# Performance work log

Measured on AMD Instinct MI355X. Metric: run time of the kernel, lower is better.

The kernel has to match this reference:

```python
import jax, jax.numpy as jnp
import numpy as np
from jax import lax

KS = 5            # patch kernel size
STRIDE = 4        # patch stride / scale ratio
SHIFTS = (2, 2)   # roll shifts before patch extraction
SOFTMAX_SCALE = 10.0
MID_CH = 64
BAND_HS = 8


def same_pad(x, k, s):
    """TensorFlow-style SAME padding for kernel k, stride s (NCHW)."""
    H, W = x.shape[-2], x.shape[-1]
    oh, ow = -(-H // s), -(-W // s)
    ph = max(0, (oh - 1) * s + k - H)
    pw = max(0, (ow - 1) * s + k - W)
    return jnp.pad(x, ((0, 0), (0, 0), (ph // 2, ph - ph // 2), (pw // 2, pw - pw // 2)))


def extract_patches(x, k, s, shifts):
    """torch.nn.Unfold equivalent with SAME padding and roll -> [N, L, C, k, k]."""
    x = same_pad(x, k, s)
    x = jnp.roll(x, shifts[0], axis=2)
    x = jnp.roll(x, shifts[1], axis=3)
    p = lax.conv_general_dilated_patches(
        x, (k, k), (s, s), 'VALID', dimension_numbers=('NCHW', 'OIHW', 'NCHW'))
    N, _, Hn, Wn = p.shape
    C = x.shape[1]
    # channel ordering is (C, kh, kw) channel-slowest, matching torch unfold
    return p.reshape(N, C, k, k, Hn * Wn).transpose(0, 4, 1, 2, 3)


def conv3(x, w, b):
    """3x3 conv, padding=1, bias + LeakyReLU(0.01) (BasicBlock)."""
    y = lax.conv_general_dilated(x, w, (1, 1), [(1, 1), (1, 1)],
                                 dimension_numbers=('NCHW', 'OIHW', 'NCHW'))
    return jax.nn.leaky_relu(y + b[None, :, None, None], 0.01)


def setup_inputs() -> dict:
    key = jax.random.key(0)
    ks = jax.random.split(key, 11)
    f32 = jnp.float32
    return {
        'ms':   jax.random.normal(ks[0], (2, BAND_HS, 96, 96), f32),
        'pan':  jax.random.normal(ks[1], (2, 1, 384, 384), f32),
        'pan2': jax.random.normal(ks[2], (2, 1, 96, 96), f32),
        'wq': jax.random.normal(ks[3], (MID_CH, 1, 3, 3), f32) * 0.1,
        'bq': jax.random.normal(ks[4], (MID_CH,), f32) * 0.02,
        'wk': jax.random.normal(ks[5], (MID_CH, 1, 3, 3), f32) * 0.1,
        'bk': jax.random.normal(ks[6], (MID_CH,), f32) * 0.02,
        'wv': jax.random.normal(ks[7], (BAND_HS, BAND_HS, 3, 3), f32) * 0.1,
        'bv': jax.random.normal(ks[8], (BAND_HS,), f32) * 0.02,
        'wr': jax.random.normal(ks[9], (BAND_HS, BAND_HS, 3, 3), f32) * 0.1,
        'br': jax.random.normal(ks[10], (BAND_HS,), f32) * 0.02,
    }


def reference(ms, pan, pan2, wq, bq, wk, bk, wv, bv, wr, br):
    k_fea = conv3(pan2, wk, bk)                       # [N, mid, h, w]
    q_fea = conv3(pan, wq, bq)                        # [N, mid, H, W]
    v_fea = conv3(ms, wv, bv)                         # [N, band, h, w]

    k_patch = extract_patches(k_fea, KS, STRIDE, SHIFTS)  # [N, L, mid, ks, ks]
    v_patch = extract_patches(v_fea, KS, STRIDE, SHIFTS)  # [N, L, band, ks, ks]

    def attend(q, kp, vp):
        # q: [mid, H, W]; kp: [L, mid, ks, ks]; vp: [L, band, ks, ks]
        norms = jnp.sqrt(jnp.sum(kp * kp, axis=(1, 2, 3)))      # per-patch L2 norms
        k0 = kp / jnp.max(norms)                                # global-max normalization
        q0 = same_pad(q[None], KS, STRIDE)                      # [1, mid, Hp, Wp]
        scores = lax.conv_general_dilated(
            q0, k0, (STRIDE, STRIDE), 'VALID',
            dimension_numbers=('NCHW', 'OIHW', 'NCHW'))          # [1, L, H', W']
        attn = jax.nn.softmax(scores * SOFTMAX_SCALE, axis=1)
        # conv_transpose2d(attn, vp, stride) == dilated conv with flipped, transposed kernel
        wT = jnp.flip(vp, (2, 3)).transpose(1, 0, 2, 3)          # [band, L, ks, ks]
        out = lax.conv_general_dilated(
            attn, wT, (1, 1), [(KS - 1, KS - 1)] * 2,
            lhs_dilation=(STRIDE, STRIDE),
            dimension_numbers=('NCHW', 'OIHW', 'NCHW'))          # [1, band, Ho, Wo]
        return out[0] / 6.0

    res = jax.vmap(attend)(q_fea, k_patch, v_patch)   # [N, band, Ho, Wo]
    return conv3(res, wr, br)
```

## Files before the change

### kernel.cpp

```cpp
#include <hip/hip_runtime.h>
#include <math.h>


typedef _Float16 f16;
typedef _Float16 f16x8 __attribute__((ext_vector_type(8)));
typedef float f32x4 __attribute__((ext_vector_type(4)));

namespace csa {
constexpr int NB   = 2;
constexpr int MID  = 64;
constexpr int BAND = 8;
constexpr int HK   = 96;
constexpr int HQ   = 384;
constexpr int HQP  = 385;
constexpr int XI   = 97;
constexpr int LN   = 24;
constexpr int L    = 576;
constexpr int LP   = 640;
constexpr int PS   = 96 * 96;
constexpr int KDIM = MID * 25;
constexpr int VDIM = BAND * 25;
constexpr int MV   = 256;
constexpr int HO   = 385;
constexpr size_t QPSN = (size_t)4 * HQP * XI * MID;

constexpr int NBQ = (NB * 4 * HQP * XI + 255) / 256;
constexpr int NBC = NB * HK * HK / 256;

constexpr size_t align256(size_t x) { return (x + 255) & ~(size_t)255; }
constexpr size_t OFF_QPS  = 0;
constexpr size_t OFF_KCL  = align256(OFF_QPS + (size_t)NB*QPSN*2);
constexpr size_t OFF_VFEA = align256(OFF_KCL + (size_t)NB*HK*HK*MID*2);
constexpr size_t OFF_SC   = align256(OFF_VFEA + (size_t)NB*BAND*HK*HK*4);
constexpr size_t OFF_KM   = align256(OFF_SC   + 256);
constexpr size_t OFF_VT   = align256(OFF_KM   + (size_t)NB*LP*KDIM*2);
constexpr size_t OFF_ST   = align256(OFF_VT   + (size_t)NB*MV*L*2);
constexpr size_t OFF_AT   = align256(OFF_ST   + (size_t)NB*PS*LP*4);
constexpr size_t OFF_D    = align256(OFF_AT   + (size_t)NB*PS*L*2);
}
using namespace csa;

__device__ __forceinline__ void dev_convq(
    const float* __restrict__ in, const float* __restrict__ w,
    const float* __restrict__ b, f16* __restrict__ out, int id) {
  int total = NB * 4 * HQP * XI;
  if (id >= total) return;
  int xi = id % XI;
  int t = id / XI;
  int yp = t % HQP;
  t /= HQP;
  int f = t % 4;
  int n = t / 4;
  int xp = 4 * xi + f;
  f16* op = out + (size_t)id * MID;
  if (yp >= HQ || xp >= HQ) {
    f16x8 z = {0, 0, 0, 0, 0, 0, 0, 0};
#pragma unroll
    for (int c8 = 0; c8 < 8; ++c8) *(f16x8*)(op + c8 * 8) = z;
    return;
  }
  const float* ip = in + (size_t)n * HQ * HQ;
  float p[9];
#pragma unroll
  for (int dy = 0; dy < 3; ++dy)
#pragma unroll
    for (int dx = 0; dx < 3; ++dx) {
      int yy = yp + dy - 1, xx = xp + dx - 1;
      p[dy * 3 + dx] = (yy >= 0 && yy < HQ && xx >= 0 && xx < HQ)
                           ? ip[(size_t)yy * HQ + xx] : 0.f;
    }
#pragma unroll
  for (int c8 = 0; c8 < 8; ++c8) {
    f16x8 o;
#pragma unroll
    for (int e = 0; e < 8; ++e) {
      int co = c8 * 8 + e;
      float acc = b[co];
#pragma unroll
      for (int k = 0; k < 9; ++k) acc = fmaf(p[k], w[co * 9 + k], acc);
      o[e] = (f16)(acc > 0.f ? acc : 0.01f * acc);
    }
    *(f16x8*)(op + c8 * 8) = o;
  }
}

__device__ __forceinline__ void dev_conv_cl(
    const float* __restrict__ in, const float* __restrict__ w,
    const float* __restrict__ b, f16* __restrict__ out, int H, int id) {
  int total = NB * H * H;
  if (id >= total) return;
  int x = id % H;
  int t = id / H;
  int y = t % H;
  int n = t / H;
  f16* op = out + (size_t)id * MID;
  const float* ip = in + (size_t)n * H * H;
  float p[9];
#pragma unroll
  for (int dy = 0; dy < 3; ++dy)
#pragma unroll
    for (int dx = 0; dx < 3; ++dx) {
      int yy = y + dy - 1, xx = x + dx - 1;
      p[dy * 3 + dx] = (yy >= 0 && yy < H && xx >= 0 && xx < H)
                           ? ip[(size_t)yy * H + xx] : 0.f;
    }
#pragma unroll
  for (int c8 = 0; c8 < 8; ++c8) {
    f16x8 o;
#pragma unroll
    for (int e = 0; e < 8; ++e) {
      int co = c8 * 8 + e;
      float acc = b[co];
#pragma unroll
      for (int k = 0; k < 9; ++k) acc = fmaf(p[k], w[co * 9 + k], acc);
      o[e] = (f16)(acc > 0.f ? acc : 0.01f * acc);
    }
    *(f16x8*)(op + c8 * 8) = o;
  }
}

__device__ __forceinline__ void dev_conv8x8(
    const float* __restrict__ in, const float* __restrict__ w,
    const float* __restrict__ b, float* __restrict__ out, int H, int W,
    int id) {
  int total = NB * H * W;
  if (id >= total) return;
  int x = id % W;
  int t = id / W;
  int y = t % H;
  int n = t / H;
  const float* ip = in + (size_t)n * BAND * H * W;
  float p[BAND][9];
#pragma unroll
  for (int ci = 0; ci < BAND; ++ci)
#pragma unroll
    for (int dy = 0; dy < 3; ++dy)
#pragma unroll
      for (int dx = 0; dx < 3; ++dx) {
        int yy = y + dy - 1, xx = x + dx - 1;
        p[ci][dy * 3 + dx] = (yy >= 0 && yy < H && xx >= 0 && xx < W)
                                 ? ip[((size_t)ci * H + yy) * W + xx] : 0.f;
      }
  float* op = out + ((size_t)n * BAND * H + y) * W + x;
  for (int co = 0; co < BAND; ++co) {
    float acc = b[co];
#pragma unroll
    for (int ci = 0; ci < BAND; ++ci)
#pragma unroll
      for (int k = 0; k < 9; ++k)
        acc = fmaf(p[ci][k], w[(co * BAND + ci) * 9 + k], acc);
    acc = acc > 0.f ? acc : 0.01f * acc;
    op[(size_t)co * H * W] = acc;
  }
}

__global__ __launch_bounds__(256) void csa_convs(
    const float* __restrict__ pan, const float* __restrict__ wq,
    const float* __restrict__ bq, f16* __restrict__ qps,
    const float* __restrict__ pan2, const float* __restrict__ wk,
    const float* __restrict__ bk, f16* __restrict__ kcl,
    const float* __restrict__ ms, const float* __restrict__ wv,
    const float* __restrict__ bv, float* __restrict__ v_fea,
    float* __restrict__ maxn2) {
  const int bid = blockIdx.x;
  const int tid = threadIdx.x;
  if (bid == 0 && tid < NB) maxn2[tid] = 0.f;
  if (bid < NBQ) {
    dev_convq(pan, wq, bq, qps, bid * 256 + tid);
  } else if (bid < NBQ + NBC) {
    dev_conv_cl(pan2, wk, bk, kcl, HK, (bid - NBQ) * 256 + tid);
  } else {
    dev_conv8x8(ms, wv, bv, v_fea, HK, HK, (bid - NBQ - NBC) * 256 + tid);
  }
}

__global__ __launch_bounds__(256) void csa_build_patches(
    const f16* __restrict__ kcl, const float* __restrict__ v_fea,
    f16* __restrict__ Kmat, f16* __restrict__ Vt, float* __restrict__ maxn2) {
  int blk = blockIdx.x;
  int n = blk / LP;
  int l = blk % LP;
  int tid = threadIdx.x;
  f16* krow = Kmat + ((size_t)n * LP + l) * KDIM;
  if (l >= L) {
    f16x8 z = {0, 0, 0, 0, 0, 0, 0, 0};
    for (int ch = tid; ch < 200; ch += 256) *(f16x8*)(krow + ch * 8) = z;
    return;
  }
  int i = l / LN, j = l % LN;
  const f16* kn = kcl + (size_t)n * HK * HK * MID;
  float ss = 0.f;
  for (int ch = tid; ch < 200; ch += 256) {
    int khkw = ch >> 3;
    int c0 = (ch & 7) * 8;
    int kh = khkw / 5, kw = khkw % 5;
    int r = (4 * i + kh + 95) % 97;
    int cc = (4 * j + kw + 95) % 97;
    f16x8 v = {0, 0, 0, 0, 0, 0, 0, 0};
    if (r < HK && cc < HK)
      v = *(const f16x8*)(kn + ((size_t)r * HK + cc) * MID + c0);
#pragma unroll
    for (int e = 0; e < 8; ++e) {
      float fv = (float)v[e];
      ss += fv * fv;
    }
    *(f16x8*)(krow + ch * 8) = v;
  }
  for (int m = tid; m < MV; m += 256) {
    float v = 0.f;
    if (m < VDIM) {
      int kw = m % 5;
      int t = m / 5;
      int kh = t % 5;
      int c = t / 5;
      int r = (4 * i + kh + 95) % 97;
      int cc = (4 * j + kw + 95) % 97;
      v = (r < HK && cc < HK)
              ? v_fea[(((size_t)n * BAND + c) * HK + r) * HK + cc] : 0.f;
    }
    Vt[((size_t)n * MV + m) * L + l] = (f16)v;
  }
  __shared__ float red[256];
  red[tid] = ss;
  __syncthreads();
  for (int s = 128; s > 0; s >>= 1) {
    if (tid < s) red[tid] += red[tid + s];
    __syncthreads();
  }
  if (tid == 0)
    atomicMax((int*)&maxn2[n], __float_as_int(red[0]));
}

__device__ __forceinline__ void gl_lds16(const f16* g, f16* s) {
  __builtin_amdgcn_global_load_lds(
      (const __attribute__((address_space(1))) void*)g,
      (__attribute__((address_space(3))) void*)s, 16, 0, 0);
}

__global__ __launch_bounds__(256) void csa_gemm1(
    const f16* __restrict__ qps, const f16* __restrict__ Km,
    float* __restrict__ C) {
  __shared__ __attribute__((aligned(16))) f16 As[3 * 4096];
  __shared__ __attribute__((aligned(16))) f16 Bs[3 * 4096];
  const int tid = threadIdx.x;
  const int w = tid >> 6;
  const int l = tid & 63;
  const int q = l >> 4;
  const int r = l & 15;

  const int flat = blockIdx.x + 5 * (blockIdx.y + 72 * blockIdx.z);
  const int logical = (flat & 7) * 90 + (flat >> 3);
  const int bx = logical % 5;
  const int by = (logical / 5) % 72;
  const int nb = logical / 360;

  qps += (size_t)nb * QPSN;
  Km += (size_t)nb * LP * KDIM;
  C += (size_t)nb * (size_t)PS * L;
  const int bm = by * 128;
  const int bn = bx * 128;
  const int wm = (w >> 1) * 64;
  const int wn = (w & 1) * 64;

  f32x4 acc[4][4];
#pragma unroll
  for (int i = 0; i < 4; ++i)
#pragma unroll
    for (int j = 0; j < 4; ++j) {
      f32x4 z = {0.f, 0.f, 0.f, 0.f};
      acc[i][j] = z;
    }

  const int pg0 = bm + w * 16;
  const int y0 = pg0 / 96, x0 = pg0 % 96;
  const int pg1 = pg0 + 64;
  const int y1 = pg1 / 96, x1 = pg1 % 96;
  const int la = r * MID + q * 8;

  const f16* gb0 = Km + (size_t)(bn + w * 16 + r) * KDIM + q * 8;
  const f16* gb1 = gb0 + (size_t)64 * KDIM;
  const int am = (w >> 1) * 4;
  const int bnn = (w & 1) * 4;

  auto stage = [&](int t, int bi) {
    f16* bA = As + bi * 4096;
    f16* bB = Bs + bi * 4096;
    const int kh = t / 10;
    const int rem = t - kh * 10;
    const int kw = rem >> 1;
    const int half = rem & 1;
    const size_t u0 =
        (((size_t)(kw & 3) * HQP + (4 * y0 + kh)) * XI + x0 + (kw >> 2)) * MID;
    const size_t u1 =
        (((size_t)(kw & 3) * HQP + (4 * y1 + kh)) * XI + x1 + (kw >> 2)) * MID;
    const size_t oA = (size_t)half * 32 + la;
    gl_lds16(qps + u0 + oA, bA + w * 512);
    gl_lds16(qps + u1 + oA, bA + 2048 + w * 512);
    gl_lds16(gb0 + (size_t)t * 32, bB + w * 512);
    gl_lds16(gb1 + (size_t)t * 32, bB + 2048 + w * 512);
  };
  auto compute = [&](int bi) {
    const f16* bA = As + bi * 4096;
    const f16* bB = Bs + bi * 4096;
    f16x8 af[4], bf[4];
#pragma unroll
    for (int u = 0; u < 4; ++u) {
      af[u] = *(const f16x8*)&bA[(am + u) * 512 + q * 128 + r * 8];
      bf[u] = *(const f16x8*)&bB[(bnn + u) * 512 + q * 128 + r * 8];
    }
#pragma unroll
    for (int i = 0; i < 4; ++i)
#pragma unroll
      for (int j = 0; j < 4; ++j)
        acc[i][j] = __builtin_amdgcn_mfma_f32_16x16x32_f16(af[i], bf[j],
                                                           acc[i][j], 0, 0, 0);
  };

  stage(0, 0);
  stage(1, 1);
  int bi = 0;
  for (int t = 0; t < 48; ++t) {
    asm volatile("s_waitcnt vmcnt(4)" ::: "memory");
    __builtin_amdgcn_s_barrier();
    __builtin_amdgcn_sched_barrier(0);
    stage(t + 2, bi == 0 ? 2 : bi - 1);
    compute(bi);
    bi = (bi == 2) ? 0 : bi + 1;
  }
  asm volatile("s_waitcnt vmcnt(4)" ::: "memory");
  __builtin_amdgcn_s_barrier();
  __builtin_amdgcn_sched_barrier(0);
  compute(bi);
  bi = (bi == 2) ? 0 : bi + 1;
  asm volatile("s_waitcnt vmcnt(0)" ::: "memory");
  __builtin_amdgcn_s_barrier();
  __builtin_amdgcn_sched_barrier(0);
  compute(bi);

  const int cn = bn + wn + r;
#pragma unroll
  for (int i = 0; i < 4; ++i) {
    int rm = bm + wm + i * 16 + q * 4;
#pragma unroll
    for (int j = 0; j < 4; ++j) {
      int c = cn + j * 16;
      if (c < L) {
#pragma unroll
        for (int rr = 0; rr < 4; ++rr)
          C[(size_t)(rm + rr) * L + c] = acc[i][j][rr];
      }
    }
  }
}

__global__ __launch_bounds__(256) void csa_gemm2(
    const f16* __restrict__ Vt, const f16* __restrict__ At,
    float* __restrict__ D) {
  __shared__ __attribute__((aligned(16))) f16 As[3 * 2048];
  __shared__ __attribute__((aligned(16))) f16 Bs[3 * 4096];
  const int tid = threadIdx.x;
  const int w = tid >> 6;
  const int l = tid & 63;
  const int q = l >> 4;
  const int r = l & 15;

  const int flat = blockIdx.x + 72 * (blockIdx.y + 4 * blockIdx.z);
  const int logical = (flat & 7) * 72 + (flat >> 3);
  const int my = logical % 4;
  const int nx = (logical / 4) % 72;
  const int nb = logical / 288;

  const f16* A = Vt + (size_t)nb * MV * L;
  const f16* Bt = At + (size_t)nb * (size_t)PS * L;
  float* C = D + (size_t)nb * (size_t)MV * PS;
  const int bm = my * 64;
  const int bn = nx * 128;
  const int wm = (w >> 1) * 32;
  const int wn = (w & 1) * 64;

  f32x4 acc[2][4];
#pragma unroll
  for (int i = 0; i < 2; ++i)
#pragma unroll
    for (int j = 0; j < 4; ++j) {
      f32x4 z = {0.f, 0.f, 0.f, 0.f};
      acc[i][j] = z;
    }

  const f16* ga  = A + (size_t)(bm + w * 16 + r) * L + q * 8;
  const f16* gb0 = Bt + (size_t)(bn + w * 16 + r) * L + q * 8;
  const f16* gb1 = gb0 + (size_t)64 * L;
  const int am = (w >> 1) * 2;
  const int bnn = (w & 1) * 4;

  auto stage = [&](int t, int bi) {
    f16* bA = As + bi * 2048;
    f16* bB = Bs + bi * 4096;
    const size_t k0 = (size_t)t * 32;
    gl_lds16(ga + k0, bA + w * 512);
    gl_lds16(gb0 + k0, bB + w * 512);
    gl_lds16(gb1 + k0, bB + 2048 + w * 512);
  };
  auto compute = [&](int bi) {
    const f16* bA = As + bi * 2048;
    const f16* bB = Bs + bi * 4096;
    f16x8 af[2], bf[4];
#pragma unroll
    for (int u = 0; u < 2; ++u)
      af[u] = *(const f16x8*)&bA[(am + u) * 512 + q * 128 + r * 8];
#pragma unroll
    for (int u = 0; u < 4; ++u)
      bf[u] = *(const f16x8*)&bB[(bnn + u) * 512 + q * 128 + r * 8];
#pragma unroll
    for (int i = 0; i < 2; ++i)
#pragma unroll
      for (int j = 0; j < 4; ++j)
        acc[i][j] = __builtin_amdgcn_mfma_f32_16x16x32_f16(af[i], bf[j],
                                                           acc[i][j], 0, 0, 0);
  };

  stage(0, 0);
  stage(1, 1);
  int bi = 0;
  for (int t = 0; t < 16; ++t) {
    asm volatile("s_waitcnt vmcnt(3)" ::: "memory");
    __builtin_amdgcn_s_barrier();
    __builtin_amdgcn_sched_barrier(0);
    stage(t + 2, bi == 0 ? 2 : bi - 1);
    compute(bi);
    bi = (bi == 2) ? 0 : bi + 1;
  }
  asm volatile("s_waitcnt vmcnt(3)" ::: "memory");
  __builtin_amdgcn_s_barrier();
  __builtin_amdgcn_sched_barrier(0);
  compute(bi);
  bi = (bi == 2) ? 0 : bi + 1;
  asm volatile("s_waitcnt vmcnt(0)" ::: "memory");
  __builtin_amdgcn_s_barrier();
  __builtin_amdgcn_sched_barrier(0);
  compute(bi);

  const int cn = bn + wn + r;
#pragma unroll
  for (int i = 0; i < 2; ++i) {
    int rm = bm + wm + i * 16 + q * 4;
#pragma unroll
    for (int j = 0; j < 4; ++j)
#pragma unroll
      for (int rr = 0; rr < 4; ++rr)
        C[(size_t)(rm + rr) * PS + cn + j * 16] = acc[i][j][rr];
  }
}

__global__ __launch_bounds__(256) void csa_softmax(
    const float* __restrict__ scoresT, const float* __restrict__ maxn2,
    f16* __restrict__ attnT) {
  const int wv = threadIdx.x >> 6;
  const int lane = threadIdx.x & 63;
  const int p = blockIdx.x * 4 + wv;
  const int n = blockIdx.y;
  const float sc = 10.f * rsqrtf(maxn2[n]);
  const float* row = scoresT + ((size_t)n * PS + p) * L;
  float v[9];
  float m = -1e30f;
#pragma unroll
  for (int j = 0; j < 9; ++j) {
    v[j] = row[lane + j * 64] * sc;
    m = fmaxf(m, v[j]);
  }
#pragma unroll
  for (int off = 32; off > 0; off >>= 1) m = fmaxf(m, __shfl_xor(m, off));
  float e[9], s = 0.f;
#pragma unroll
  for (int j = 0; j < 9; ++j) {
    e[j] = __expf(v[j] - m);
    s += e[j];
  }
#pragma unroll
  for (int off = 32; off > 0; off >>= 1) s += __shfl_xor(s, off);
  const float inv = 1.f / s;
  f16* orow = attnT + ((size_t)n * PS + p) * L;
#pragma unroll
  for (int j = 0; j < 9; ++j) orow[lane + j * 64] = (f16)(e[j] * inv);
}

__global__ __launch_bounds__(256) void csa_gather_conv(
    const float* __restrict__ D, const float* __restrict__ wr,
    const float* __restrict__ br, float* __restrict__ out) {
  __shared__ float rs[BAND][18][18];
  __shared__ float wsm[BAND * BAND * 9];
  __shared__ float brs[BAND];
  const int tid = threadIdx.x;
  const int n = blockIdx.z;
  const int ty = blockIdx.y, tx = blockIdx.x;
  const float* Dn = D + (size_t)n * MV * PS;

  for (int i = tid; i < BAND * BAND * 9; i += 256) wsm[i] = wr[i];
  if (tid < BAND) brs[tid] = br[tid];

  for (int idx = tid; idx < BAND * 18 * 18; idx += 256) {
    int ci = idx / 324;
    int rem = idx - ci * 324;
    int yy = rem / 18;
    int xx = rem - yy * 18;
    int oy = ty * 16 - 1 + yy;
    int ox = tx * 16 - 1 + xx;
    float s = 0.f;
    if (oy >= 0 && oy < HO && ox >= 0 && ox < HO) {
      int kh0 = oy & 3;
      int kw0 = ox & 3;
      for (int kh = kh0; kh < 5; kh += 4) {
        int y = (oy - kh) >> 2;
        if (y < 0 || y >= 96) continue;
        for (int kw = kw0; kw < 5; kw += 4) {
          int x = (ox - kw) >> 2;
          if (x < 0 || x >= 96) continue;
          s += Dn[(size_t)(ci * 25 + kh * 5 + kw) * PS + y * 96 + x];
        }
      }
      s *= (1.f / 6.f);
    }
    rs[ci][yy][xx] = s;
  }
  __syncthreads();

  const int y = tid >> 4, x = tid & 15;
  const int oy = ty * 16 + y, ox = tx * 16 + x;
  if (oy >= HO || ox >= HO) return;
  float p[BAND][9];
#pragma unroll
  for (int ci = 0; ci < BAND; ++ci)
#pragma unroll
    for (int dy = 0; dy < 3; ++dy)
#pragma unroll
      for (int dx = 0; dx < 3; ++dx)
        p[ci][dy * 3 + dx] = rs[ci][y + dy][x + dx];
  float* op = out + ((size_t)n * BAND * HO + oy) * HO + ox;
  for (int co = 0; co < BAND; ++co) {
    float acc = brs[co];
#pragma unroll
    for (int ci = 0; ci < BAND; ++ci)
#pragma unroll
      for (int k = 0; k < 9; ++k)
        acc = fmaf(p[ci][k], wsm[(co * BAND + ci) * 9 + k], acc);
    acc = acc > 0.f ? acc : 0.01f * acc;
    op[(size_t)co * HO * HO] = acc;
  }
}

extern "C" void kernel_launch(void* const* d_in, const int* in_sizes, int n_in,
                              void* d_out, int out_size, void* d_ws,
                              size_t ws_size, hipStream_t stream) {
  const float* ms   = (const float*)d_in[0];
  const float* pan  = (const float*)d_in[1];
  const float* pan2 = (const float*)d_in[2];
  const float* wq = (const float*)d_in[3];
  const float* bq = (const float*)d_in[4];
  const float* wk = (const float*)d_in[5];
  const float* bk = (const float*)d_in[6];
  const float* wv = (const float*)d_in[7];
  const float* bv = (const float*)d_in[8];
  const float* wr = (const float*)d_in[9];
  const float* br = (const float*)d_in[10];
  float* out = (float*)d_out;

  char* ws = (char*)d_ws;
  f16*   qps   = (f16*)(ws + OFF_QPS);
  f16*   kcl   = (f16*)(ws + OFF_KCL);
  float* v_fea = (float*)(ws + OFF_VFEA);
  float* maxn2 = (float*)(ws + OFF_SC);
  f16*   Kmat  = (f16*)(ws + OFF_KM);
  f16*   Vt    = (f16*)(ws + OFF_VT);
  float* scoT  = (float*)(ws + OFF_ST);
  f16*   attnT = (f16*)(ws + OFF_AT);
  float* Dm    = (float*)(ws + OFF_D);

  dim3 b256(256);
  csa_convs<<<dim3(NBQ + 2 * NBC), b256, 0, stream>>>(
      pan, wq, bq, qps, pan2, wk, bk, kcl, ms, wv, bv, v_fea, maxn2);
  csa_build_patches<<<dim3(NB * LP), b256, 0, stream>>>(kcl, v_fea, Kmat, Vt,
                                                        maxn2);

  csa_gemm1<<<dim3(LP / 128, PS / 128, NB), b256, 0, stream>>>(qps, Kmat,
                                                               scoT);

  csa_softmax<<<dim3(PS / 4, NB), b256, 0, stream>>>(scoT, maxn2, attnT);

  csa_gemm2<<<dim3(PS / 128, MV / 64, NB), b256, 0, stream>>>(Vt, attnT, Dm);

  csa_gather_conv<<<dim3((HO + 15) / 16, (HO + 15) / 16, NB), b256, 0,
                    stream>>>(Dm, wr, br, out);
}
```

Baseline: 281.9 us.

## Fuse softmax exponentiation into second GEMM using precomputed row statistics

Replaces the softmax kernel that wrote a full f16 attention matrix with a kernel that stores only per-row max and inverse sum. The second GEMM now loads fp32 scores into registers, computes exp and converts to f16 while staging into LDS, and applies the 1/sum normalisation in the epilogue. This removes the write and re-read of the attention intermediate, but gemm2 now reads twice-as-wide fp32 data and recomputes exp for each row-block tile, with a register-staged pipeline.

```diff
diff --git a/kernel.cpp b/kernel.cpp
--- a/kernel.cpp
+++ b/kernel.cpp
@@ -35,8 +35,8 @@
 constexpr size_t OFF_KM   = align256(OFF_SC   + 256);
 constexpr size_t OFF_VT   = align256(OFF_KM   + (size_t)NB*LP*KDIM*2);
 constexpr size_t OFF_ST   = align256(OFF_VT   + (size_t)NB*MV*L*2);
-constexpr size_t OFF_AT   = align256(OFF_ST   + (size_t)NB*PS*LP*4);
-constexpr size_t OFF_D    = align256(OFF_AT   + (size_t)NB*PS*L*2);
+constexpr size_t OFF_RS   = align256(OFF_ST   + (size_t)NB*PS*LP*4);
+constexpr size_t OFF_D    = align256(OFF_RS   + (size_t)NB*PS*8);
 }
 using namespace csa;
 
@@ -353,108 +353,9 @@
   }
 }
 
-__global__ __launch_bounds__(256) void csa_gemm2(
-    const f16* __restrict__ Vt, const f16* __restrict__ At,
-    float* __restrict__ D) {
-  __shared__ __attribute__((aligned(16))) f16 As[3 * 2048];
-  __shared__ __attribute__((aligned(16))) f16 Bs[3 * 4096];
-  const int tid = threadIdx.x;
-  const int w = tid >> 6;
-  const int l = tid & 63;
-  const int q = l >> 4;
-  const int r = l & 15;
-
-  const int flat = blockIdx.x + 72 * (blockIdx.y + 4 * blockIdx.z);
-  const int logical = (flat & 7) * 72 + (flat >> 3);
-  const int my = logical % 4;
-  const int nx = (logical / 4) % 72;
-  const int nb = logical / 288;
-
-  const f16* A = Vt + (size_t)nb * MV * L;
-  const f16* Bt = At + (size_t)nb * (size_t)PS * L;
-  float* C = D + (size_t)nb * (size_t)MV * PS;
-  const int bm = my * 64;
-  const int bn = nx * 128;
-  const int wm = (w >> 1) * 32;
-  const int wn = (w & 1) * 64;
-
-  f32x4 acc[2][4];
-#pragma unroll
-  for (int i = 0; i < 2; ++i)
-#pragma unroll
-    for (int j = 0; j < 4; ++j) {
-      f32x4 z = {0.f, 0.f, 0.f, 0.f};
-      acc[i][j] = z;
-    }
-
-  const f16* ga  = A + (size_t)(bm + w * 16 + r) * L + q * 8;
-  const f16* gb0 = Bt + (size_t)(bn + w * 16 + r) * L + q * 8;
-  const f16* gb1 = gb0 + (size_t)64 * L;
-  const int am = (w >> 1) * 2;
-  const int bnn = (w & 1) * 4;
-
-  auto stage = [&](int t, int bi) {
-    f16* bA = As + bi * 2048;
-    f16* bB = Bs + bi * 4096;
-    const size_t k0 = (size_t)t * 32;
-    gl_lds16(ga + k0, bA + w * 512);
-    gl_lds16(gb0 + k0, bB + w * 512);
-    gl_lds16(gb1 + k0, bB + 2048 + w * 512);
-  };
-  auto compute = [&](int bi) {
-    const f16* bA = As + bi * 2048;
-    const f16* bB = Bs + bi * 4096;
-    f16x8 af[2], bf[4];
-#pragma unroll
-    for (int u = 0; u < 2; ++u)
-      af[u] = *(const f16x8*)&bA[(am + u) * 512 + q * 128 + r * 8];
-#pragma unroll
-    for (int u = 0; u < 4; ++u)
-      bf[u] = *(const f16x8*)&bB[(bnn + u) * 512 + q * 128 + r * 8];
-#pragma unroll
-    for (int i = 0; i < 2; ++i)
-#pragma unroll
-      for (int j = 0; j < 4; ++j)
-        acc[i][j] = __builtin_amdgcn_mfma_f32_16x16x32_f16(af[i], bf[j],
-                                                           acc[i][j], 0, 0, 0);
-  };
-
-  stage(0, 0);
-  stage(1, 1);
-  int bi = 0;
-  for (int t = 0; t < 16; ++t) {
-    asm volatile("s_waitcnt vmcnt(3)" ::: "memory");
-    __builtin_amdgcn_s_barrier();
-    __builtin_amdgcn_sched_barrier(0);
-    stage(t + 2, bi == 0 ? 2 : bi - 1);
-    compute(bi);
-    bi = (bi == 2) ? 0 : bi + 1;
-  }
-  asm volatile("s_waitcnt vmcnt(3)" ::: "memory");
-  __builtin_amdgcn_s_barrier();
-  __builtin_amdgcn_sched_barrier(0);
-  compute(bi);
-  bi = (bi == 2) ? 0 : bi + 1;
-  asm volatile("s_waitcnt vmcnt(0)" ::: "memory");
-  __builtin_amdgcn_s_barrier();
-  __builtin_amdgcn_sched_barrier(0);
-  compute(bi);
-
-  const int cn = bn + wn + r;
-#pragma unroll
-  for (int i = 0; i < 2; ++i) {
-    int rm = bm + wm + i * 16 + q * 4;
-#pragma unroll
-    for (int j = 0; j < 4; ++j)
-#pragma unroll
-      for (int rr = 0; rr < 4; ++rr)
-        C[(size_t)(rm + rr) * PS + cn + j * 16] = acc[i][j][rr];
-  }
-}
-
-__global__ __launch_bounds__(256) void csa_softmax(
+__global__ __launch_bounds__(256) void csa_rowstats(
     const float* __restrict__ scoresT, const float* __restrict__ maxn2,
-    f16* __restrict__ attnT) {
+    float2* __restrict__ rowst) {
   const int wv = threadIdx.x >> 6;
   const int lane = threadIdx.x & 63;
   const int p = blockIdx.x * 4 + wv;
@@ -470,18 +371,163 @@
   }
 #pragma unroll
   for (int off = 32; off > 0; off >>= 1) m = fmaxf(m, __shfl_xor(m, off));
-  float e[9], s = 0.f;
-#pragma unroll
-  for (int j = 0; j < 9; ++j) {
-    e[j] = __expf(v[j] - m);
-    s += e[j];
-  }
+  float s = 0.f;
+#pragma unroll
+  for (int j = 0; j < 9; ++j) s += __expf(v[j] - m);
 #pragma unroll
   for (int off = 32; off > 0; off >>= 1) s += __shfl_xor(s, off);
-  const float inv = 1.f / s;
-  f16* orow = attnT + ((size_t)n * PS + p) * L;
-#pragma unroll
-  for (int j = 0; j < 9; ++j) orow[lane + j * 64] = (f16)(e[j] * inv);
+  if (lane == 0) rowst[(size_t)n * PS + p] = make_float2(m, 1.f / s);
+}
+
+__global__ __launch_bounds__(256) void csa_gemm2f(
+    const f16* __restrict__ Vt, const float* __restrict__ scoT,
+    const float* __restrict__ maxn2, const float2* __restrict__ rowst,
+    float* __restrict__ D) {
+  __shared__ __attribute__((aligned(16))) f16 As[3 * 2048];
+  __shared__ __attribute__((aligned(16))) f16 Bs[3 * 4096];
+  const int tid = threadIdx.x;
+  const int w = tid >> 6;
+  const int lid = tid & 63;
+  const int q = lid >> 4;
+  const int r = lid & 15;
+
+  const int flat = blockIdx.x + 72 * (blockIdx.y + 4 * blockIdx.z);
+  const int logical = (flat & 7) * 72 + (flat >> 3);
+  const int my = logical % 4;
+  const int nx = (logical / 4) % 72;
+  const int nb = logical / 288;
+
+  const f16* A = Vt + (size_t)nb * MV * L;
+  const float* Sc = scoT + (size_t)nb * (size_t)PS * L;
+  const float2* rs = rowst + (size_t)nb * PS;
+  float* C = D + (size_t)nb * (size_t)MV * PS;
+  const int bm = my * 64;
+  const int bn = nx * 128;
+  const int wm = (w >> 1) * 32;
+  const int wn = (w & 1) * 64;
+  const float sc = 10.f * rsqrtf(maxn2[nb]);
+
+  const int prow0 = bn + w * 16 + r;
+  const float m0 = rs[prow0].x;
+  const float m1 = rs[prow0 + 64].x;
+  const float* bsrc0 = Sc + (size_t)prow0 * L + q * 8;
+
+  f32x4 acc[2][4];
+#pragma unroll
+  for (int i = 0; i < 2; ++i)
+#pragma unroll
+    for (int j = 0; j < 4; ++j) {
+      f32x4 z = {0.f, 0.f, 0.f, 0.f};
+      acc[i][j] = z;
+    }
+
+  const f16* ga = A + (size_t)(bm + w * 16 + r) * L + q * 8;
+  const int am = (w >> 1) * 2;
+  const int bnn = (w & 1) * 4;
+
+#define BLOAD_(T, RG)                                              \
+  {                                                                \
+    const float* p0_ = bsrc0 + (T) * 32;                           \
+    RG[0] = *(const f32x4*)p0_;                                    \
+    RG[1] = *(const f32x4*)(p0_ + 4);                              \
+    const float* p1_ = p0_ + (size_t)64 * L;                       \
+    RG[2] = *(const f32x4*)p1_;                                    \
+    RG[3] = *(const f32x4*)(p1_ + 4);                              \
+  }
+
+#define BWRITE_(T, RG)                                             \
+  {                                                                \
+    f16* bB_ = Bs + ((T) % 3) * 4096;                              \
+    f16x8 o0_, o1_;                                                \
+    _Pragma("unroll") for (int e_ = 0; e_ < 4; ++e_) {             \
+      o0_[e_]     = (f16)__expf(RG[0][e_] * sc - m0);              \
+      o0_[4 + e_] = (f16)__expf(RG[1][e_] * sc - m0);              \
+      o1_[e_]     = (f16)__expf(RG[2][e_] * sc - m1);              \
+      o1_[4 + e_] = (f16)__expf(RG[3][e_] * sc - m1);              \
+    }                                                              \
+    *(f16x8*)(bB_ + w * 512 + lid * 8) = o0_;                      \
+    *(f16x8*)(bB_ + 2048 + w * 512 + lid * 8) = o1_;               \
+  }
+
+  auto glldsA = [&](int t) {
+    gl_lds16(ga + (size_t)t * 32, As + (t % 3) * 2048 + w * 512);
+  };
+  auto compute = [&](int bi) {
+    const f16* bA = As + bi * 2048;
+    const f16* bB = Bs + bi * 4096;
+    f16x8 af[2], bf[4];
+#pragma unroll
+    for (int u = 0; u < 2; ++u)
+      af[u] = *(const f16x8*)&bA[(am + u) * 512 + q * 128 + r * 8];
+#pragma unroll
+    for (int u = 0; u < 4; ++u)
+      bf[u] = *(const f16x8*)&bB[(bnn + u) * 512 + q * 128 + r * 8];
+#pragma unroll
+    for (int i = 0; i < 2; ++i)
+#pragma unroll
+      for (int j = 0; j < 4; ++j)
+        acc[i][j] = __builtin_amdgcn_mfma_f32_16x16x32_f16(af[i], bf[j],
+                                                           acc[i][j], 0, 0, 0);
+  };
+
+  f32x4 rg0[4], rg1[4], rg2[4];
+
+  BLOAD_(0, rg0);
+  glldsA(0);
+  BLOAD_(1, rg1);
+  glldsA(1);
+  BLOAD_(2, rg2);
+  asm volatile("s_waitcnt vmcnt(10)" ::: "memory");
+  BWRITE_(0, rg0);
+
+#define ITER_(T, RGCONS, RGLOAD)                                   \
+  {                                                                \
+    asm volatile("s_waitcnt vmcnt(5) lgkmcnt(0)" ::: "memory");    \
+    __builtin_amdgcn_s_barrier();                                  \
+    __builtin_amdgcn_sched_barrier(0);                             \
+    BLOAD_((T) + 3, RGLOAD);                                       \
+    glldsA((T) + 2);                                               \
+    BWRITE_((T) + 1, RGCONS);                                      \
+    compute((T) % 3);                                              \
+  }
+
+  for (int tt = 0; tt < 5; ++tt) {
+    const int t0 = tt * 3;
+    ITER_(t0 + 0, rg1, rg0);
+    ITER_(t0 + 1, rg2, rg1);
+    ITER_(t0 + 2, rg0, rg2);
+  }
+  asm volatile("s_waitcnt vmcnt(5) lgkmcnt(0)" ::: "memory");
+  __builtin_amdgcn_s_barrier();
+  __builtin_amdgcn_sched_barrier(0);
+  glldsA(17);
+  BWRITE_(16, rg1);
+  compute(15 % 3);
+  asm volatile("s_waitcnt vmcnt(1) lgkmcnt(0)" ::: "memory");
+  __builtin_amdgcn_s_barrier();
+  __builtin_amdgcn_sched_barrier(0);
+  BWRITE_(17, rg2);
+  compute(16 % 3);
+  asm volatile("s_waitcnt vmcnt(0) lgkmcnt(0)" ::: "memory");
+  __builtin_amdgcn_s_barrier();
+  __builtin_amdgcn_sched_barrier(0);
+  compute(17 % 3);
+
+  const int cn = bn + wn + r;
+#pragma unroll
+  for (int j = 0; j < 4; ++j) {
+    const float iz = rs[cn + j * 16].y;
+#pragma unroll
+    for (int i = 0; i < 2; ++i) {
+      int rm = bm + wm + i * 16 + q * 4;
+#pragma unroll
+      for (int rr = 0; rr < 4; ++rr)
+        C[(size_t)(rm + rr) * PS + cn + j * 16] = acc[i][j][rr] * iz;
+    }
+  }
+#undef ITER_
+#undef BLOAD_
+#undef BWRITE_
 }
 
 __global__ __launch_bounds__(256) void csa_gather_conv(
@@ -565,15 +611,15 @@
   float* out = (float*)d_out;
 
   char* ws = (char*)d_ws;
-  f16*   qps   = (f16*)(ws + OFF_QPS);
-  f16*   kcl   = (f16*)(ws + OFF_KCL);
-  float* v_fea = (float*)(ws + OFF_VFEA);
-  float* maxn2 = (float*)(ws + OFF_SC);
-  f16*   Kmat  = (f16*)(ws + OFF_KM);
-  f16*   Vt    = (f16*)(ws + OFF_VT);
-  float* scoT  = (float*)(ws + OFF_ST);
-  f16*   attnT = (f16*)(ws + OFF_AT);
-  float* Dm    = (float*)(ws + OFF_D);
+  f16*    qps   = (f16*)(ws + OFF_QPS);
+  f16*    kcl   = (f16*)(ws + OFF_KCL);
+  float*  v_fea = (float*)(ws + OFF_VFEA);
+  float*  maxn2 = (float*)(ws + OFF_SC);
+  f16*    Kmat  = (f16*)(ws + OFF_KM);
+  f16*    Vt    = (f16*)(ws + OFF_VT);
+  float*  scoT  = (float*)(ws + OFF_ST);
+  float2* rowst = (float2*)(ws + OFF_RS);
+  float*  Dm    = (float*)(ws + OFF_D);
 
   dim3 b256(256);
   csa_convs<<<dim3(NBQ + 2 * NBC), b256, 0, stream>>>(
@@ -584,9 +630,10 @@
   csa_gemm1<<<dim3(LP / 128, PS / 128, NB), b256, 0, stream>>>(qps, Kmat,
                                                                scoT);
 
-  csa_softmax<<<dim3(PS / 4, NB), b256, 0, stream>>>(scoT, maxn2, attnT);
-
-  csa_gemm2<<<dim3(PS / 128, MV / 64, NB), b256, 0, stream>>>(Vt, attnT, Dm);
+  csa_rowstats<<<dim3(PS / 4, NB), b256, 0, stream>>>(scoT, maxn2, rowst);
+
+  csa_gemm2f<<<dim3(PS / 128, MV / 64, NB), b256, 0, stream>>>(
+      Vt, scoT, maxn2, rowst, Dm);
 
   csa_gather_conv<<<dim3((HO + 15) / 16, (HO + 15) / 16, NB), b256, 0,
                     stream>>>(Dm, wr, br, out);
```

Measured after the change: 293.2 us. 4.0% more time.
